# Kernel optimization log

Measured on AMD Instinct MI355X. Metric: run time of the kernel, lower is better.

Reference implementation:

```python
import jax, jax.numpy as jnp
import numpy as np

NUM_HEADS = 32
HEAD_DIM = 128  # 4096 / 32


def setup_inputs() -> dict:
    key = jax.random.key(0)
    k1, k2, k3 = jax.random.split(key, 3)
    B, S, H = 1, 2048, 4096
    hidden_states = jax.random.normal(k1, (B, S, H), dtype=jnp.float32)
    # causal additive mask, broadcast over heads: 0 on/below diagonal, large negative above
    neg = jnp.finfo(jnp.float32).min
    causal = jnp.triu(jnp.full((S, S), neg, dtype=jnp.float32), k=1)
    attention_mask = causal[None, None, :, :]  # [1,1,S,S]
    w_pack = jax.random.normal(k2, (3 * H, H), dtype=jnp.float32) * 0.02
    w_o = jax.random.normal(k3, (H, H), dtype=jnp.float32) * 0.02
    return {"hidden_states": hidden_states, "attention_mask": attention_mask,
            "w_pack": w_pack, "w_o": w_o}


def reference(hidden_states, attention_mask, w_pack, w_o):
    B, S, H = hidden_states.shape
    nh, hd = NUM_HEADS, HEAD_DIM
    # fused QKV projection (Linear, no bias): x @ W^T
    proj = hidden_states @ w_pack.T                      # [B,S,3H]
    q, k, v = jnp.split(proj, 3, axis=-1)
    q = q.reshape(B, S, nh, hd).transpose(0, 2, 1, 3)    # [B,nh,S,hd]
    k = k.reshape(B, S, nh, hd).transpose(0, 2, 1, 3)
    v = v.reshape(B, S, nh, hd).transpose(0, 2, 1, 3)
    scale = 1.0 / jnp.sqrt(jnp.float32(hd))
    attn = jnp.einsum('bhqd,bhkd->bhqk', q, k) * scale   # [B,nh,S,S]
    attn = attn + attention_mask
    attn = jnp.maximum(attn, jnp.finfo(attn.dtype).min)  # clamp like torch.max(..., finfo.min)
    attn = jax.nn.softmax(attn, axis=-1)
    out = jnp.einsum('bhqk,bhkd->bhqd', attn, v)         # [B,nh,S,hd]
    out = out.transpose(0, 2, 1, 3).reshape(B, S, nh * hd)
    return out @ w_o.T                                    # [B,S,H]
```

## Files before the change

### kernel.cpp

```cpp
#include <hip/hip_runtime.h>
#include <stdint.h>

typedef __attribute__((ext_vector_type(8))) short short8;
typedef __attribute__((ext_vector_type(4))) float floatx4;

#define SEQ    2048
#define HID    4096
#define NHEAD  32
#define HDIMV  128
#define PROJN  12288

__device__ __forceinline__ unsigned short f2bf(float f) {
  union { float f; unsigned u; } v; v.f = f;
  unsigned r = (v.u + 0x7fffu + ((v.u >> 16) & 1u)) >> 16;
  return (unsigned short)r;
}

__device__ __forceinline__ void g2l16(const void* g, void* l) {
  __builtin_amdgcn_global_load_lds(
      (const __attribute__((address_space(1))) void*)g,
      (__attribute__((address_space(3))) void*)l, 16, 0, 0);
}

__global__ __launch_bounds__(256) void pack_fp32(const float* __restrict__ src,
                                                 unsigned short* __restrict__ dst, int K,
                                                 int scale_rows, float scale) {
  const int rp = blockIdx.x, kt = blockIdx.y, t = threadIdx.x;
  const long tb = ((long)rp * gridDim.y + kt) * 8192;
#pragma unroll
  for (int j = 0; j < 4; j++) {
    int ch = t + j * 256;
    int r = ch & 127, cc = ch >> 7;
    float sc = (rp * 128 + r < scale_rows) ? scale : 1.0f;
    const float* s = src + (long)(rp * 128 + r) * K + kt * 64 + cc * 8;
    float4 a = *(const float4*)s;
    float4 b = *(const float4*)(s + 4);
    short8 o;
    o[0] = (short)f2bf(a.x * sc); o[1] = (short)f2bf(a.y * sc);
    o[2] = (short)f2bf(a.z * sc); o[3] = (short)f2bf(a.w * sc);
    o[4] = (short)f2bf(b.x * sc); o[5] = (short)f2bf(b.y * sc);
    o[6] = (short)f2bf(b.z * sc); o[7] = (short)f2bf(b.w * sc);
    *(short8*)(dst + tb + ch * 8) = o;
  }
}

__global__ __launch_bounds__(256) void pack_qk(const unsigned short* __restrict__ proj,
                                               unsigned short* __restrict__ dstQ,
                                               unsigned short* __restrict__ dstK) {
  const int st = blockIdx.x, h = blockIdx.y, t = threadIdx.x;
  const long tb = ((long)(h * 16 + st)) * 16384;
#pragma unroll
  for (int j = 0; j < 8; j++) {
    int ch = t + j * 256;
    int r = ch & 127, cc = ch >> 7;
    long so = (long)(st * 128 + r) * PROJN + h * 128 + cc * 8;
    *(short8*)(dstQ + tb + ch * 8) = *(const short8*)(proj + so);
    *(short8*)(dstK + tb + ch * 8) = *(const short8*)(proj + so + HID);
  }
}

__global__ __launch_bounds__(256) void pack_v(const unsigned short* __restrict__ proj,
                                              unsigned short* __restrict__ Vf) {
  __shared__ unsigned short T[128 * 136];
  const int st = blockIdx.x, h = blockIdx.y, t = threadIdx.x;
  const long tb = ((long)(h * 16 + st)) * 16384;
  const unsigned short* src = proj + (long)(st * 128) * PROJN + 2 * HID + h * 128;
#pragma unroll
  for (int it = 0; it < 8; it++) {
    int idx = t * 8 + it * 2048;
    int r = idx >> 7, c = idx & 127;
    *(short8*)(T + r * 136 + c) = *(const short8*)(src + (long)r * PROJN + c);
  }
  __syncthreads();
#pragma unroll
  for (int pass = 0; pass < 4; pass++) {
    int d = (t >> 3) + pass * 32;
    int sc = t & 7;
    short8 lo, hi;
#pragma unroll
    for (int j = 0; j < 8; j++) lo[j] = (short)T[(sc * 16 + j) * 136 + d];
#pragma unroll
    for (int j = 0; j < 8; j++) hi[j] = (short)T[(sc * 16 + 8 + j) * 136 + d];
    *(short8*)(Vf + tb + ((sc * 2) * 128 + d) * 8) = lo;
    *(short8*)(Vf + tb + ((sc * 2 + 1) * 128 + d) * 8) = hi;
  }
}

template<int OUT_F32>
__global__ __launch_bounds__(256, 4) void gemm_pk(
    const unsigned short* __restrict__ Ap,
    const unsigned short* __restrict__ Bp,
    void* __restrict__ C, int N, int K) {
  __shared__ __align__(16) unsigned short As[8192];
  __shared__ __align__(16) unsigned short Bs[8192];
  const int t = threadIdx.x;
  const int wave = t >> 6, lane = t & 63;
  const int bid = blockIdx.x;
  const int xcd = bid & 7;
  const int li = bid >> 3;
  const int mi = li & 15;
  const int ni = (li >> 4) * 8 + xcd;
  const int KT = K >> 6;
  const unsigned short* at = Ap + (long)mi * KT * 8192 + t * 8;
  const unsigned short* bt = Bp + (long)ni * KT * 8192 + t * 8;
  unsigned short* asl = As + wave * 512;
  unsigned short* bsl = Bs + wave * 512;

  const int mw = (wave >> 1) * 64;
  const int nw = (wave & 1) * 64;
  const int lq = lane & 15, lg = lane >> 4;

  floatx4 zero = {0.f, 0.f, 0.f, 0.f};
  floatx4 acc[4][4];
  for (int i = 0; i < 4; i++)
    for (int j = 0; j < 4; j++) acc[i][j] = zero;

  for (int kt = 0; kt < KT; kt++) {
    __syncthreads();
    const unsigned short* ak = at + (long)kt * 8192;
    const unsigned short* bk = bt + (long)kt * 8192;
#pragma unroll
    for (int j = 0; j < 4; j++) g2l16(ak + j * 2048, asl + j * 2048);
#pragma unroll
    for (int j = 0; j < 4; j++) g2l16(bk + j * 2048, bsl + j * 2048);
    __syncthreads();
#pragma unroll
    for (int kk = 0; kk < 2; kk++) {
      const int ch = (kk * 4 + lg) * 1024;
      short8 af[4], bfr[4];
#pragma unroll
      for (int i = 0; i < 4; i++)
        af[i] = *(const short8*)(As + ch + (mw + i * 16 + lq) * 8);
#pragma unroll
      for (int j = 0; j < 4; j++)
        bfr[j] = *(const short8*)(Bs + ch + (nw + j * 16 + lq) * 8);
#pragma unroll
      for (int i = 0; i < 4; i++)
#pragma unroll
        for (int j = 0; j < 4; j++)
          acc[i][j] = __builtin_amdgcn_mfma_f32_16x16x32_bf16(af[i], bfr[j], acc[i][j], 0, 0, 0);
    }
  }

  const int row0 = mi * 128 + mw + lg * 4;
  const int col0 = ni * 128 + nw + lq;
  if (OUT_F32) {
    float* Cf = (float*)C;
#pragma unroll
    for (int i = 0; i < 4; i++)
#pragma unroll
      for (int j = 0; j < 4; j++)
#pragma unroll
        for (int r = 0; r < 4; r++)
          Cf[(long)(row0 + i * 16 + r) * N + col0 + j * 16] = acc[i][j][r];
  } else {
    unsigned short* Cb = (unsigned short*)C;
#pragma unroll
    for (int i = 0; i < 4; i++)
#pragma unroll
      for (int j = 0; j < 4; j++)
#pragma unroll
        for (int r = 0; r < 4; r++)
          Cb[(long)(row0 + i * 16 + r) * N + col0 + j * 16] = f2bf(acc[i][j][r]);
  }
}

__device__ __forceinline__ void stage_tile(const unsigned short* g, unsigned short* lds,
                                           int wave, int lane) {
  const unsigned short* gp = g + wave * 4096 + lane * 8;
  unsigned short* lp = lds + wave * 4096;
#pragma unroll
  for (int j = 0; j < 8; j++) g2l16(gp + j * 512, lp + j * 512);
}

__global__ __launch_bounds__(256, 1) void attn_kernel(
    const unsigned short* __restrict__ Qf,
    const unsigned short* __restrict__ Kf,
    const unsigned short* __restrict__ Vf,
    unsigned short* __restrict__ aop) {
  __shared__ __align__(16) unsigned short Ks[2][16384];
  __shared__ __align__(16) unsigned short Vs[2][16384];
  __shared__ __align__(16) unsigned short Ps[16384];
  const int bx = blockIdx.x;
  const int h = bx & 31;
  const int qt = 15 - (bx >> 5);
  const int t = threadIdx.x, wave = t >> 6, lane = t & 63;
  const int lq = lane & 15, lg = lane >> 4;
  const int wOff = wave * 32;

  const unsigned short* qb = Qf + ((long)(h * 16 + qt)) * 16384;
  short8 qf[2][4];
#pragma unroll
  for (int i = 0; i < 2; i++)
#pragma unroll
    for (int kk = 0; kk < 4; kk++)
      qf[i][kk] = *(const short8*)(qb + ((kk * 4 + lg) * 128 + wOff + i * 16 + lq) * 8);

  float mraw[2][4], lsum[2][4];
  floatx4 zero = {0.f, 0.f, 0.f, 0.f};
  floatx4 o[2][8];
#pragma unroll
  for (int i = 0; i < 2; i++)
#pragma unroll
    for (int r = 0; r < 4; r++) { mraw[i][r] = -INFINITY; lsum[i][r] = 0.f; }
#pragma unroll
  for (int i = 0; i < 2; i++)
#pragma unroll
    for (int j = 0; j < 8; j++) o[i][j] = zero;

  const unsigned short* kb0 = Kf + ((long)h * 16) * 16384;
  const unsigned short* vb0 = Vf + ((long)h * 16) * 16384;
  stage_tile(kb0, Ks[0], wave, lane);
  stage_tile(vb0, Vs[0], wave, lane);

  for (int kv = 0; kv <= qt; kv++) {
    const int cur = kv & 1;
    const bool diag = (kv == qt);
    __syncthreads();
    if (!diag) {
      stage_tile(kb0 + (long)(kv + 1) * 16384, Ks[1 - cur], wave, lane);
      stage_tile(vb0 + (long)(kv + 1) * 16384, Vs[1 - cur], wave, lane);
    }

    floatx4 s[2][8];
#pragma unroll
    for (int i = 0; i < 2; i++)
#pragma unroll
      for (int j = 0; j < 8; j++) s[i][j] = zero;
#pragma unroll
    for (int kk = 0; kk < 4; kk++) {
      short8 bfr[8];
#pragma unroll
      for (int j = 0; j < 8; j++)
        bfr[j] = *(const short8*)(&Ks[cur][((kk * 4 + lg) * 128 + j * 16 + lq) * 8]);
#pragma unroll
      for (int i = 0; i < 2; i++)
#pragma unroll
        for (int j = 0; j < 8; j++)
          s[i][j] = __builtin_amdgcn_mfma_f32_16x16x32_bf16(qf[i][kk], bfr[j], s[i][j], 0, 0, 0);
    }

    if (diag) {
#pragma unroll
      for (int i = 0; i < 2; i++)
#pragma unroll
        for (int r = 0; r < 4; r++) {
          int qrow = qt * 128 + wOff + i * 16 + lg * 4 + r;
#pragma unroll
          for (int j = 0; j < 8; j++)
            if (kv * 128 + j * 16 + lq > qrow) s[i][j][r] = -INFINITY;
        }
    }

    float alpha_[2][4];
#pragma unroll
    for (int i = 0; i < 2; i++) {
#pragma unroll
      for (int r = 0; r < 4; r++) {
        float mx = s[i][0][r];
#pragma unroll
        for (int j = 1; j < 8; j++) mx = fmaxf(mx, s[i][j][r]);
#pragma unroll
        for (int d = 1; d < 16; d <<= 1) mx = fmaxf(mx, __shfl_xor(mx, d, 64));
        float mnew = fmaxf(mraw[i][r], mx);
        float al = exp2f(mraw[i][r] - mnew);
        float ps = 0.f;
#pragma unroll
        for (int j = 0; j < 8; j++) {
          float p = exp2f(s[i][j][r] - mnew);
          s[i][j][r] = p;
          ps += p;
        }
#pragma unroll
        for (int d = 1; d < 16; d <<= 1) ps += __shfl_xor(ps, d, 64);
        lsum[i][r] = lsum[i][r] * al + ps;
        mraw[i][r] = mnew;
        alpha_[i][r] = al;
      }
    }
#pragma unroll
    for (int i = 0; i < 2; i++)
#pragma unroll
      for (int j = 0; j < 8; j++)
#pragma unroll
        for (int r = 0; r < 4; r++) o[i][j][r] *= alpha_[i][r];

#pragma unroll
    for (int i = 0; i < 2; i++)
#pragma unroll
      for (int r = 0; r < 4; r++) {
        int prow = wOff + i * 16 + lg * 4 + r;
#pragma unroll
        for (int j = 0; j < 8; j++)
          Ps[((j * 2 + (lq >> 3)) * 128 + prow) * 8 + (lq & 7)] = f2bf(s[i][j][r]);
      }

#pragma unroll
    for (int kk = 0; kk < 4; kk++) {
      short8 pf[2], vf[8];
#pragma unroll
      for (int i = 0; i < 2; i++)
        pf[i] = *(const short8*)(Ps + ((kk * 4 + lg) * 128 + wOff + i * 16 + lq) * 8);
#pragma unroll
      for (int j = 0; j < 8; j++)
        vf[j] = *(const short8*)(&Vs[cur][((kk * 4 + lg) * 128 + j * 16 + lq) * 8]);
#pragma unroll
      for (int i = 0; i < 2; i++)
#pragma unroll
        for (int j = 0; j < 8; j++)
          o[i][j] = __builtin_amdgcn_mfma_f32_16x16x32_bf16(pf[i], vf[j], o[i][j], 0, 0, 0);
    }
  }

#pragma unroll
  for (int i = 0; i < 2; i++) {
    float inv[4];
#pragma unroll
    for (int r = 0; r < 4; r++) inv[r] = 1.0f / lsum[i][r];
#pragma unroll
    for (int r = 0; r < 4; r++) {
      int prow = wOff + i * 16 + lg * 4 + r;
#pragma unroll
      for (int j = 0; j < 8; j++)
        Ps[((j * 2 + (lq >> 3)) * 128 + prow) * 8 + (lq & 7)] = f2bf(o[i][j][r] * inv[r]);
    }
  }
#pragma unroll
  for (int it = 0; it < 8; it++) {
    int row_loc = it * 4 + (lane >> 4);
    int cc = lane & 15;
    short8 v = *(const short8*)(Ps + (cc * 128 + wOff + row_loc) * 8);
    long tb = ((long)qt * 64 + h * 2 + (cc >> 3)) * 8192;
    *(short8*)(aop + tb + ((cc & 7) * 128 + wOff + row_loc) * 8) = v;
  }
}

extern "C" void kernel_launch(void* const* d_in, const int* in_sizes, int n_in,
                              void* d_out, int out_size, void* d_ws, size_t ws_size,
                              hipStream_t stream) {
  (void)in_sizes; (void)n_in; (void)out_size;
  const float* hs = (const float*)d_in[0];
  const float* wp = (const float*)d_in[2];
  const float* wo = (const float*)d_in[3];
  float* out = (float*)d_out;
  char* ws = (char*)d_ws;

  unsigned short* Ap1  = (unsigned short*)(ws);
  unsigned short* Bp1  = (unsigned short*)(ws + 16777216);
  unsigned short* Bp2  = (unsigned short*)(ws + 117440512);
  unsigned short* proj = (unsigned short*)(ws + 150994944);
  unsigned short* aop  = (unsigned short*)(ws + 201326592);
  unsigned short* Qf   = (unsigned short*)(ws);
  unsigned short* Kf   = (unsigned short*)(ws + 16777216);
  unsigned short* Vf   = (unsigned short*)(ws + 33554432);
  if (ws_size < 218103808) return;

  pack_fp32<<<dim3(16, 64), 256, 0, stream>>>(hs, Ap1, HID, 0, 1.0f);
  pack_fp32<<<dim3(96, 64), 256, 0, stream>>>(wp, Bp1, HID, 4096, 0.12751744154f);
  pack_fp32<<<dim3(32, 64), 256, 0, stream>>>(wo, Bp2, HID, 0, 1.0f);

  gemm_pk<0><<<1536, 256, 0, stream>>>(Ap1, Bp1, (void*)proj, PROJN, HID);

  pack_qk<<<dim3(16, 32), 256, 0, stream>>>(proj, Qf, Kf);
  pack_v<<<dim3(16, 32), 256, 0, stream>>>(proj, Vf);

  attn_kernel<<<512, 256, 0, stream>>>(Qf, Kf, Vf, aop);

  gemm_pk<1><<<512, 256, 0, stream>>>(aop, Bp2, (void*)out, HID, HID);
}
```

Baseline: 780.9 us.

## Read K/V fragments directly from global memory and run two blocks per CU

Removes the double-buffered LDS staging of K and V tiles and the per-iteration barrier, so each wave loads its MFMA operand fragments straight from global memory (relying on L2 and cache reuse). With LDS use cut to the P buffer, launch bounds rise to two blocks per CU for more latency hiding. The block-to-query-tile mapping is changed to interleave long and short causal rows, and s_setprio wraps the MFMA bursts. The risk is redundant global traffic and exposed load latency, since each wave now refetches the same K/V data that was previously shared through LDS.

After: 901.6 us. 1.15x slower.

```diff
diff --git a/kernel.cpp b/kernel.cpp
--- a/kernel.cpp
+++ b/kernel.cpp
@@ -165,25 +165,16 @@
   }
 }
 
-__device__ __forceinline__ void stage_tile(const unsigned short* g, unsigned short* lds,
-                                           int wave, int lane) {
-  const unsigned short* gp = g + wave * 4096 + lane * 8;
-  unsigned short* lp = lds + wave * 4096;
-#pragma unroll
-  for (int j = 0; j < 8; j++) g2l16(gp + j * 512, lp + j * 512);
-}
-
-__global__ __launch_bounds__(256, 1) void attn_kernel(
+__global__ __launch_bounds__(256, 2) void attn_kernel(
     const unsigned short* __restrict__ Qf,
     const unsigned short* __restrict__ Kf,
     const unsigned short* __restrict__ Vf,
     unsigned short* __restrict__ aop) {
-  __shared__ __align__(16) unsigned short Ks[2][16384];
-  __shared__ __align__(16) unsigned short Vs[2][16384];
   __shared__ __align__(16) unsigned short Ps[16384];
   const int bx = blockIdx.x;
   const int h = bx & 31;
-  const int qt = 15 - (bx >> 5);
+  const int idx = bx >> 5;
+  const int qt = (idx < 8) ? (15 - idx) : (idx - 8);
   const int t = threadIdx.x, wave = t >> 6, lane = t & 63;
   const int lq = lane & 15, lg = lane >> 4;
   const int wOff = wave * 32;
@@ -210,17 +201,11 @@
 
   const unsigned short* kb0 = Kf + ((long)h * 16) * 16384;
   const unsigned short* vb0 = Vf + ((long)h * 16) * 16384;
-  stage_tile(kb0, Ks[0], wave, lane);
-  stage_tile(vb0, Vs[0], wave, lane);
 
   for (int kv = 0; kv <= qt; kv++) {
-    const int cur = kv & 1;
     const bool diag = (kv == qt);
-    __syncthreads();
-    if (!diag) {
-      stage_tile(kb0 + (long)(kv + 1) * 16384, Ks[1 - cur], wave, lane);
-      stage_tile(vb0 + (long)(kv + 1) * 16384, Vs[1 - cur], wave, lane);
-    }
+    const unsigned short* kb = kb0 + (long)kv * 16384;
+    const unsigned short* vb = vb0 + (long)kv * 16384;
 
     floatx4 s[2][8];
 #pragma unroll
@@ -232,12 +217,14 @@
       short8 bfr[8];
 #pragma unroll
       for (int j = 0; j < 8; j++)
-        bfr[j] = *(const short8*)(&Ks[cur][((kk * 4 + lg) * 128 + j * 16 + lq) * 8]);
+        bfr[j] = *(const short8*)(kb + ((kk * 4 + lg) * 128 + j * 16 + lq) * 8);
+      __builtin_amdgcn_s_setprio(1);
 #pragma unroll
       for (int i = 0; i < 2; i++)
 #pragma unroll
         for (int j = 0; j < 8; j++)
           s[i][j] = __builtin_amdgcn_mfma_f32_16x16x32_bf16(qf[i][kk], bfr[j], s[i][j], 0, 0, 0);
+      __builtin_amdgcn_s_setprio(0);
     }
 
     if (diag) {
@@ -303,12 +290,14 @@
         pf[i] = *(const short8*)(Ps + ((kk * 4 + lg) * 128 + wOff + i * 16 + lq) * 8);
 #pragma unroll
       for (int j = 0; j < 8; j++)
-        vf[j] = *(const short8*)(&Vs[cur][((kk * 4 + lg) * 128 + j * 16 + lq) * 8]);
+        vf[j] = *(const short8*)(vb + ((kk * 4 + lg) * 128 + j * 16 + lq) * 8);
+      __builtin_amdgcn_s_setprio(1);
 #pragma unroll
       for (int i = 0; i < 2; i++)
 #pragma unroll
         for (int j = 0; j < 8; j++)
           o[i][j] = __builtin_amdgcn_mfma_f32_16x16x32_bf16(pf[i], vf[j], o[i][j], 0, 0, 0);
+      __builtin_amdgcn_s_setprio(0);
     }
   }
 
```

## Fuse Q/K/V repacking into the QKV projection GEMM epilogue

Applied to the files above, without the earlier changes.

Adds a dedicated QKV GEMM whose epilogue writes bf16 results directly into the packed Q, K and transposed V layouts used by the attention kernel. This removes the intermediate proj buffer and the two repacking kernels along with their extra global memory round trip and launches. The epilogue now does scattered 2-byte stores that are less coalesced than the original row-major writes, which may slow the GEMM's store phase.

Result: no change. 776.5 us (-0.6%).

```diff
diff --git a/kernel.cpp b/kernel.cpp
--- a/kernel.cpp
+++ b/kernel.cpp
@@ -41,48 +41,6 @@
     o[4] = (short)f2bf(b.x * sc); o[5] = (short)f2bf(b.y * sc);
     o[6] = (short)f2bf(b.z * sc); o[7] = (short)f2bf(b.w * sc);
     *(short8*)(dst + tb + ch * 8) = o;
-  }
-}
-
-__global__ __launch_bounds__(256) void pack_qk(const unsigned short* __restrict__ proj,
-                                               unsigned short* __restrict__ dstQ,
-                                               unsigned short* __restrict__ dstK) {
-  const int st = blockIdx.x, h = blockIdx.y, t = threadIdx.x;
-  const long tb = ((long)(h * 16 + st)) * 16384;
-#pragma unroll
-  for (int j = 0; j < 8; j++) {
-    int ch = t + j * 256;
-    int r = ch & 127, cc = ch >> 7;
-    long so = (long)(st * 128 + r) * PROJN + h * 128 + cc * 8;
-    *(short8*)(dstQ + tb + ch * 8) = *(const short8*)(proj + so);
-    *(short8*)(dstK + tb + ch * 8) = *(const short8*)(proj + so + HID);
-  }
-}
-
-__global__ __launch_bounds__(256) void pack_v(const unsigned short* __restrict__ proj,
-                                              unsigned short* __restrict__ Vf) {
-  __shared__ unsigned short T[128 * 136];
-  const int st = blockIdx.x, h = blockIdx.y, t = threadIdx.x;
-  const long tb = ((long)(h * 16 + st)) * 16384;
-  const unsigned short* src = proj + (long)(st * 128) * PROJN + 2 * HID + h * 128;
-#pragma unroll
-  for (int it = 0; it < 8; it++) {
-    int idx = t * 8 + it * 2048;
-    int r = idx >> 7, c = idx & 127;
-    *(short8*)(T + r * 136 + c) = *(const short8*)(src + (long)r * PROJN + c);
-  }
-  __syncthreads();
-#pragma unroll
-  for (int pass = 0; pass < 4; pass++) {
-    int d = (t >> 3) + pass * 32;
-    int sc = t & 7;
-    short8 lo, hi;
-#pragma unroll
-    for (int j = 0; j < 8; j++) lo[j] = (short)T[(sc * 16 + j) * 136 + d];
-#pragma unroll
-    for (int j = 0; j < 8; j++) hi[j] = (short)T[(sc * 16 + 8 + j) * 136 + d];
-    *(short8*)(Vf + tb + ((sc * 2) * 128 + d) * 8) = lo;
-    *(short8*)(Vf + tb + ((sc * 2 + 1) * 128 + d) * 8) = hi;
   }
 }
 
@@ -165,6 +123,92 @@
   }
 }
 
+__global__ __launch_bounds__(256, 4) void gemm_qkv(
+    const unsigned short* __restrict__ Ap,
+    const unsigned short* __restrict__ Bp,
+    unsigned short* __restrict__ Qf,
+    unsigned short* __restrict__ Kf,
+    unsigned short* __restrict__ Vf) {
+  __shared__ __align__(16) unsigned short As[8192];
+  __shared__ __align__(16) unsigned short Bs[8192];
+  const int t = threadIdx.x;
+  const int wave = t >> 6, lane = t & 63;
+  const int bid = blockIdx.x;
+  const int xcd = bid & 7;
+  const int li = bid >> 3;
+  const int mi = li & 15;
+  const int ni = (li >> 4) * 8 + xcd;
+  const int KT = HID >> 6;
+  const unsigned short* at = Ap + (long)mi * KT * 8192 + t * 8;
+  const unsigned short* bt = Bp + (long)ni * KT * 8192 + t * 8;
+  unsigned short* asl = As + wave * 512;
+  unsigned short* bsl = Bs + wave * 512;
+
+  const int mw = (wave >> 1) * 64;
+  const int nw = (wave & 1) * 64;
+  const int lq = lane & 15, lg = lane >> 4;
+
+  floatx4 zero = {0.f, 0.f, 0.f, 0.f};
+  floatx4 acc[4][4];
+  for (int i = 0; i < 4; i++)
+    for (int j = 0; j < 4; j++) acc[i][j] = zero;
+
+  for (int kt = 0; kt < KT; kt++) {
+    __syncthreads();
+    const unsigned short* ak = at + (long)kt * 8192;
+    const unsigned short* bk = bt + (long)kt * 8192;
+#pragma unroll
+    for (int j = 0; j < 4; j++) g2l16(ak + j * 2048, asl + j * 2048);
+#pragma unroll
+    for (int j = 0; j < 4; j++) g2l16(bk + j * 2048, bsl + j * 2048);
+    __syncthreads();
+#pragma unroll
+    for (int kk = 0; kk < 2; kk++) {
+      const int ch = (kk * 4 + lg) * 1024;
+      short8 af[4], bfr[4];
+#pragma unroll
+      for (int i = 0; i < 4; i++)
+        af[i] = *(const short8*)(As + ch + (mw + i * 16 + lq) * 8);
+#pragma unroll
+      for (int j = 0; j < 4; j++)
+        bfr[j] = *(const short8*)(Bs + ch + (nw + j * 16 + lq) * 8);
+#pragma unroll
+      for (int i = 0; i < 4; i++)
+#pragma unroll
+        for (int j = 0; j < 4; j++)
+          acc[i][j] = __builtin_amdgcn_mfma_f32_16x16x32_bf16(af[i], bfr[j], acc[i][j], 0, 0, 0);
+    }
+  }
+
+  const int sec = ni >> 5;
+  const int h = ni & 31;
+  unsigned short* dst =
+      (sec == 0 ? Qf : (sec == 1 ? Kf : Vf)) + ((long)(h * 16 + mi)) * 16384;
+  if (sec < 2) {
+#pragma unroll
+    for (int i = 0; i < 4; i++)
+#pragma unroll
+      for (int j = 0; j < 4; j++)
+#pragma unroll
+        for (int r = 0; r < 4; r++) {
+          int row = mw + i * 16 + lg * 4 + r;
+          int c = nw + j * 16 + lq;
+          dst[((c >> 3) * 128 + row) * 8 + (c & 7)] = f2bf(acc[i][j][r]);
+        }
+  } else {
+#pragma unroll
+    for (int i = 0; i < 4; i++)
+#pragma unroll
+      for (int j = 0; j < 4; j++)
+#pragma unroll
+        for (int r = 0; r < 4; r++) {
+          int s = mw + i * 16 + lg * 4 + r;
+          int d = nw + j * 16 + lq;
+          dst[((s >> 3) * 128 + d) * 8 + (s & 7)] = f2bf(acc[i][j][r]);
+        }
+  }
+}
+
 __device__ __forceinline__ void stage_tile(const unsigned short* g, unsigned short* lds,
                                            int wave, int lane) {
   const unsigned short* gp = g + wave * 4096 + lane * 8;
@@ -345,24 +389,20 @@
   float* out = (float*)d_out;
   char* ws = (char*)d_ws;
 
-  unsigned short* Ap1  = (unsigned short*)(ws);
-  unsigned short* Bp1  = (unsigned short*)(ws + 16777216);
-  unsigned short* Bp2  = (unsigned short*)(ws + 117440512);
-  unsigned short* proj = (unsigned short*)(ws + 150994944);
-  unsigned short* aop  = (unsigned short*)(ws + 201326592);
-  unsigned short* Qf   = (unsigned short*)(ws);
-  unsigned short* Kf   = (unsigned short*)(ws + 16777216);
-  unsigned short* Vf   = (unsigned short*)(ws + 33554432);
+  unsigned short* Ap1 = (unsigned short*)(ws);
+  unsigned short* Bp1 = (unsigned short*)(ws + 16777216);
+  unsigned short* Bp2 = (unsigned short*)(ws + 117440512);
+  unsigned short* Qf  = (unsigned short*)(ws + 150994944);
+  unsigned short* Kf  = (unsigned short*)(ws + 167772160);
+  unsigned short* Vf  = (unsigned short*)(ws + 184549376);
+  unsigned short* aop = (unsigned short*)(ws + 201326592);
   if (ws_size < 218103808) return;
 
   pack_fp32<<<dim3(16, 64), 256, 0, stream>>>(hs, Ap1, HID, 0, 1.0f);
   pack_fp32<<<dim3(96, 64), 256, 0, stream>>>(wp, Bp1, HID, 4096, 0.12751744154f);
   pack_fp32<<<dim3(32, 64), 256, 0, stream>>>(wo, Bp2, HID, 0, 1.0f);
 
-  gemm_pk<0><<<1536, 256, 0, stream>>>(Ap1, Bp1, (void*)proj, PROJN, HID);
-
-  pack_qk<<<dim3(16, 32), 256, 0, stream>>>(proj, Qf, Kf);
-  pack_v<<<dim3(16, 32), 256, 0, stream>>>(proj, Vf);
+  gemm_qkv<<<1536, 256, 0, stream>>>(Ap1, Bp1, Qf, Kf, Vf);
 
   attn_kernel<<<512, 256, 0, stream>>>(Qf, Kf, Vf, aop);
 
```
